# Performance work log

Hardware: AMD Instinct MI355X
Metric: run time of the kernel (lower is better)

Reference implementation:

```python
import jax, jax.numpy as jnp
import numpy as np

EPS = 1e-12  # torch F.normalize eps

def _l2norm(x):
    n = jnp.sqrt(jnp.sum(x * x, axis=-1, keepdims=True))
    return x / jnp.maximum(n, EPS)

def setup_inputs() -> dict:
    key = jax.random.key(0)
    k1, k2 = jax.random.split(key)
    B, C, H, W = 4, 256, 48, 48
    qkv = jax.random.normal(k1, (B, 3 * C, H, W), dtype=jnp.float32)
    temp = jnp.ones((8, 1, 1), dtype=jnp.float32)
    proj_w = jax.random.normal(k2, (C, C), dtype=jnp.float32) * (1.0 / np.sqrt(C))
    proj_b = jnp.zeros((C,), dtype=jnp.float32)
    return {"qkv": qkv, "temp": temp, "proj_w": proj_w, "proj_b": proj_b, "h": H, "w": W}

def reference(qkv, temp, proj_w, proj_b, h, w):
    num_heads = temp.shape[0]
    b = qkv.shape[0]
    q, k, v = jnp.split(qkv, 3, axis=1)

    def to_heads(x):
        # b (head c) h w -> b head (h w) c
        return x.reshape(b, num_heads, -1, h * w).transpose(0, 1, 3, 2)

    q = _l2norm(to_heads(q))
    k = _l2norm(to_heads(k))
    v = to_heads(v)

    # [b, head, N, N], temp (head,1,1) broadcasts over (n, m)
    attn = jnp.einsum('bhnc,bhmc->bhnm', q, k) * temp
    attn = jax.nn.softmax(jax.nn.relu(attn), axis=-1)
    out = jnp.einsum('bhnm,bhmc->bhnc', attn, v)
    # b head N c -> b head c N -> b (head c) h w
    out = out.transpose(0, 1, 3, 2).reshape(b, -1, h, w)
    # 1x1 conv == channel matmul
    out = jnp.einsum('oc,bchw->bohw', proj_w, out) + proj_b[None, :, None, None]
    return out
```

## Files before the change

### kernel.cpp

```cpp
#include <hip/hip_runtime.h>

typedef unsigned short u16;
typedef unsigned int   u32;
typedef __attribute__((ext_vector_type(8))) short short8;
typedef __attribute__((ext_vector_type(4))) float f32x4;

#define NB    4
#define NCH   256
#define NHD   8
#define HD    32
#define NSP   2304
#define NBH   32
#define NKT   36
#define KPW   9

__device__ __forceinline__ u16 f2bf(float f) {
    u32 u = __float_as_uint(f);
    u += 0x7FFFu + ((u >> 16) & 1u);
    return (u16)(u >> 16);
}
__device__ __forceinline__ u32 pack2(float a, float b) {
    return (u32)f2bf(a) | ((u32)f2bf(b) << 16);
}
__device__ __forceinline__ u32 pkfast(float a, float b) {
#if __has_builtin(__builtin_amdgcn_cvt_pk_bf16_f32)
    typedef __attribute__((ext_vector_type(2))) __bf16 bf2;
    union { bf2 v; u32 u; } cv;
    cv.v = __builtin_amdgcn_cvt_pk_bf16_f32(a, b);
    return cv.u;
#else
    return __builtin_amdgcn_perm(__float_as_uint(b), __float_as_uint(a), 0x07060302u);
#endif
}
__device__ __forceinline__ float fexp2(float x) {
#if __has_builtin(__builtin_amdgcn_exp2f)
    return __builtin_amdgcn_exp2f(x);
#else
    return exp2f(x);
#endif
}

__global__ __launch_bounds__(192) void prep_kernel(
    const float* __restrict__ qkv, const float* __restrict__ temp,
    const float* __restrict__ projw,
    u16* __restrict__ Qn, u16* __restrict__ Kn, u16* __restrict__ Vp,
    u16* __restrict__ Wb)
{
    const int p  = blockIdx.y;
    const int bh = blockIdx.z, b = bh >> 3, head = bh & 7;

    if (p == 3) {
        const int idx = (bh * 6 + blockIdx.x) * 192 + threadIdx.x;
        if (idx < NCH * NCH / 4) {
            float4 v = ((const float4*)projw)[idx];
            ((uint2*)Wb)[idx] = make_uint2(pack2(v.x, v.y), pack2(v.z, v.w));
        }
        return;
    }

    const int i  = blockIdx.x * 192 + threadIdx.x;
    const int n0 = i * 2;
    const float* src = qkv + ((size_t)(b * 3 * NCH + p * NCH + head * HD)) * NSP + n0;

    float2 v[HD];
#pragma unroll
    for (int d = 0; d < HD; ++d) v[d] = *(const float2*)(src + (size_t)d * NSP);

    if (p == 2) {
        const int tile = n0 >> 6, loc = n0 & 63;
        const int c = loc >> 5, r5 = loc & 31;
        const int qd  = (r5 < 16) ? (r5 >> 2) : ((r5 - 16) >> 2);
        const int jj  = (r5 < 16) ? (r5 & 3) : (4 + (r5 & 3));
        u16* dst = Vp + (size_t)bh * NSP * HD + (size_t)tile * 2048 + c * 32 + qd * 8 + jj;
#pragma unroll
        for (int d = 0; d < HD; ++d) *(u32*)(dst + d * 64) = pack2(v[d].x, v[d].y);
    } else {
        float s0 = 0.f, s1 = 0.f;
#pragma unroll
        for (int d = 0; d < HD; ++d) { s0 += v[d].x * v[d].x; s1 += v[d].y * v[d].y; }
        float sc0 = 1.f / fmaxf(sqrtf(s0), 1e-12f);
        float sc1 = 1.f / fmaxf(sqrtf(s1), 1e-12f);
        if (p == 0) {
            const float t = temp[head] * 1.44269504088896f;
            sc0 *= t; sc1 *= t;
        }
        u32 pk[HD];
#pragma unroll
        for (int j = 0; j < HD / 2; ++j) pk[j]          = pack2(v[2 * j].x * sc0, v[2 * j + 1].x * sc0);
#pragma unroll
        for (int j = 0; j < HD / 2; ++j) pk[HD / 2 + j] = pack2(v[2 * j].y * sc1, v[2 * j + 1].y * sc1);
        u16* dst = (p == 0 ? Qn : Kn) + ((size_t)bh * NSP + n0) * HD;
#pragma unroll
        for (int j = 0; j < 8; ++j) ((uint4*)dst)[j] = ((const uint4*)pk)[j];
    }
}

__global__ __launch_bounds__(256) void attn_kernel(
    const u16* __restrict__ Qn, const u16* __restrict__ Kn,
    const u16* __restrict__ Vp, u16* __restrict__ X)
{
    __shared__ float cmb[4][64][25];
    const int bh = blockIdx.x, b = bh >> 3, head = bh & 7;
    const int w = threadIdx.x >> 6, lane = threadIdx.x & 63;
    const int l15 = lane & 15, quad = lane >> 4;
    const int qbase = blockIdx.y * 64;

    const u16* Kg = Kn + (size_t)bh * NSP * HD + (size_t)w * KPW * 2048 + l15 * HD + quad * 8;
    const u16* Vg = Vp + (size_t)bh * NSP * HD + (size_t)w * KPW * 2048 + l15 * 64 + quad * 8;

    short8 qf[4];
#pragma unroll
    for (int t2 = 0; t2 < 4; ++t2)
        qf[t2] = *(const short8*)(Qn + ((size_t)bh * NSP + qbase + t2 * 16 + l15) * HD + quad * 8);

    const short one = (short)0x3F80;
    const short8 vones = {one, one, one, one, one, one, one, one};
    const f32x4 zf = {0.f, 0.f, 0.f, 0.f};

    f32x4 oacc[4][2] = {{{0,0,0,0},{0,0,0,0}},{{0,0,0,0},{0,0,0,0}},
                        {{0,0,0,0},{0,0,0,0}},{{0,0,0,0},{0,0,0,0}}};
    f32x4 rsac[4]    = {{0,0,0,0},{0,0,0,0},{0,0,0,0},{0,0,0,0}};

    short8 ka[4];
#pragma unroll
    for (int i = 0; i < 4; ++i) ka[i] = *(const short8*)(Kg + i * 512);

    for (int kt = 0; kt < KPW; ++kt) {
        short8 vb[2][2];
#pragma unroll
        for (int c = 0; c < 2; ++c)
#pragma unroll
            for (int h = 0; h < 2; ++h)
                vb[c][h] = *(const short8*)(Vg + (size_t)kt * 2048 + h * 1024 + c * 32);
        short8 kan[4];
        if (kt + 1 < KPW) {
            const u16* Kp2 = Kg + (size_t)(kt + 1) * 2048;
#pragma unroll
            for (int i = 0; i < 4; ++i) kan[i] = *(const short8*)(Kp2 + i * 512);
        }

#pragma unroll
        for (int t2 = 0; t2 < 4; ++t2) {
            f32x4 sf[4];
#pragma unroll
            for (int i = 0; i < 4; ++i)
                sf[i] = __builtin_amdgcn_mfma_f32_16x16x32_bf16(ka[i], qf[t2], zf, 0, 0, 0);
            u32 pk[4][2];
#pragma unroll
            for (int i = 0; i < 4; ++i) {
                pk[i][0] = pkfast(fexp2(fmaxf(sf[i][0], 0.f)), fexp2(fmaxf(sf[i][1], 0.f)));
                pk[i][1] = pkfast(fexp2(fmaxf(sf[i][2], 0.f)), fexp2(fmaxf(sf[i][3], 0.f)));
            }
#pragma unroll
            for (int c = 0; c < 2; ++c) {
                union { short8 s; u32 u[4]; } pa;
                pa.u[0] = pk[2 * c][0];     pa.u[1] = pk[2 * c][1];
                pa.u[2] = pk[2 * c + 1][0]; pa.u[3] = pk[2 * c + 1][1];
                oacc[t2][0] = __builtin_amdgcn_mfma_f32_16x16x32_bf16(pa.s, vb[c][0], oacc[t2][0], 0, 0, 0);
                oacc[t2][1] = __builtin_amdgcn_mfma_f32_16x16x32_bf16(pa.s, vb[c][1], oacc[t2][1], 0, 0, 0);
                rsac[t2]    = __builtin_amdgcn_mfma_f32_16x16x32_bf16(pa.s, vones,    rsac[t2],    0, 0, 0);
            }
        }

        if (kt + 1 < KPW) {
#pragma unroll
            for (int i = 0; i < 4; ++i) ka[i] = kan[i];
        }
    }

#pragma unroll
    for (int pass = 0; pass < 2; ++pass) {
        if (pass) __syncthreads();
        {
            float* my = &cmb[w][lane][0];
#pragma unroll
            for (int tt = 0; tt < 2; ++tt) {
                const int t2 = pass * 2 + tt;
#pragma unroll
                for (int h = 0; h < 2; ++h)
#pragma unroll
                    for (int r = 0; r < 4; ++r) my[tt * 12 + h * 4 + r] = oacc[t2][h][r];
#pragma unroll
                for (int r = 0; r < 4; ++r) my[tt * 12 + 8 + r] = rsac[t2][r];
            }
        }
        __syncthreads();
        if ((w >> 1) == pass) {
            const int t2 = w;
            const int tt = w & 1;
            float o0[4] = {0,0,0,0}, o1[4] = {0,0,0,0}, rsum[4] = {0,0,0,0};
#pragma unroll
            for (int j = 0; j < 4; ++j) {
                const float* srcp = &cmb[j][lane][tt * 12];
#pragma unroll
                for (int r = 0; r < 4; ++r) {
                    o0[r]   += srcp[r];
                    o1[r]   += srcp[4 + r];
                    rsum[r] += srcp[8 + r];
                }
            }
            u16* Xb = X + (size_t)b * NSP * NCH + head * HD;
#pragma unroll
            for (int r = 0; r < 4; ++r) {
                const float inv = 1.f / rsum[r];
                u16* row = Xb + (size_t)(qbase + t2 * 16 + quad * 4 + r) * NCH;
                row[l15]      = f2bf(o0[r] * inv);
                row[16 + l15] = f2bf(o1[r] * inv);
            }
        }
    }
}

__global__ __launch_bounds__(256) void proj_kernel(
    const u16* __restrict__ Wb, const u16* __restrict__ X,
    const float* __restrict__ bias, float* __restrict__ out)
{
    const int b = blockIdx.z;
    const int w = threadIdx.x >> 6, lane = threadIdx.x & 63;
    const int l15 = lane & 15, quad = lane >> 4;
    const int obase = blockIdx.y * 64 + w * 16;
    const int nbase = blockIdx.x * 32;

    const u16* wrow = Wb + (size_t)(obase + l15) * NCH + quad * 8;
    const u16* xrow = X + ((size_t)b * NSP + nbase + l15) * NCH + quad * 8;

    f32x4 acc[2] = {{0,0,0,0},{0,0,0,0}};
#pragma unroll
    for (int ks = 0; ks < 8; ++ks) {
        const short8 af = *(const short8*)(wrow + ks * 32);
        acc[0] = __builtin_amdgcn_mfma_f32_16x16x32_bf16(af, *(const short8*)(xrow + ks * 32), acc[0], 0, 0, 0);
        acc[1] = __builtin_amdgcn_mfma_f32_16x16x32_bf16(af, *(const short8*)(xrow + (size_t)16 * NCH + ks * 32), acc[1], 0, 0, 0);
    }
#pragma unroll
    for (int r = 0; r < 4; ++r) {
        const int o = obase + quad * 4 + r;
        const float bo = bias[o];
        float* orow = out + ((size_t)b * NCH + o) * NSP + nbase;
        orow[l15]      = acc[0][r] + bo;
        orow[16 + l15] = acc[1][r] + bo;
    }
}

extern "C" void kernel_launch(void* const* d_in, const int* in_sizes, int n_in,
                              void* d_out, int out_size, void* d_ws, size_t ws_size,
                              hipStream_t stream) {
    const float* qkv   = (const float*)d_in[0];
    const float* temp  = (const float*)d_in[1];
    const float* projw = (const float*)d_in[2];
    const float* projb = (const float*)d_in[3];
    float* out = (float*)d_out;

    u16* Qn = (u16*)d_ws;
    u16* Kn = Qn + (size_t)NBH * NSP * HD;
    u16* Vp = Kn + (size_t)NBH * NSP * HD;
    u16* X  = Vp + (size_t)NBH * NSP * HD;
    u16* Wb = X + (size_t)NB * NSP * NCH;

    prep_kernel<<<dim3(6, 4, NBH), dim3(192), 0, stream>>>(qkv, temp, projw, Qn, Kn, Vp, Wb);
    attn_kernel<<<dim3(NBH, NSP / 64), dim3(256), 0, stream>>>(Qn, Kn, Vp, X);
    proj_kernel<<<dim3(NSP / 32, NCH / 64, NB), dim3(256), 0, stream>>>(Wb, X, projb, out);
}
```

Baseline: 151.2 us.

## Split attention waves into query-pair by key-half instead of four key splits

```diff
diff --git a/kernel.cpp b/kernel.cpp
--- a/kernel.cpp
+++ b/kernel.cpp
@@ -12,7 +12,7 @@
 #define NSP   2304
 #define NBH   32
 #define NKT   36
-#define KPW   9
+#define KPW   18
 
 __device__ __forceinline__ u16 f2bf(float f) {
     u32 u = __float_as_uint(f);
@@ -39,6 +39,7 @@
     return exp2f(x);
 #endif
 }
+__device__ __forceinline__ float er(float x) { return fexp2(fmaxf(x, 0.f)); }
 
 __global__ __launch_bounds__(192) void prep_kernel(
     const float* __restrict__ qkv, const float* __restrict__ temp,
@@ -104,22 +105,22 @@
     const int w = threadIdx.x >> 6, lane = threadIdx.x & 63;
     const int l15 = lane & 15, quad = lane >> 4;
     const int qbase = blockIdx.y * 64;
-
-    const u16* Kg = Kn + (size_t)bh * NSP * HD + (size_t)w * KPW * 2048 + l15 * HD + quad * 8;
-    const u16* Vg = Vp + (size_t)bh * NSP * HD + (size_t)w * KPW * 2048 + l15 * 64 + quad * 8;
-
-    short8 qf[4];
-#pragma unroll
-    for (int t2 = 0; t2 < 4; ++t2)
-        qf[t2] = *(const short8*)(Qn + ((size_t)bh * NSP + qbase + t2 * 16 + l15) * HD + quad * 8);
+    const int qpair = w >> 1, khalf = w & 1;
+
+    const u16* Kg = Kn + (size_t)bh * NSP * HD + (size_t)khalf * KPW * 2048 + l15 * HD + quad * 8;
+    const u16* Vg = Vp + (size_t)bh * NSP * HD + (size_t)khalf * KPW * 2048 + l15 * 64 + quad * 8;
+
+    short8 qf[2];
+#pragma unroll
+    for (int t = 0; t < 2; ++t)
+        qf[t] = *(const short8*)(Qn + ((size_t)bh * NSP + qbase + (qpair * 2 + t) * 16 + l15) * HD + quad * 8);
 
     const short one = (short)0x3F80;
     const short8 vones = {one, one, one, one, one, one, one, one};
     const f32x4 zf = {0.f, 0.f, 0.f, 0.f};
 
-    f32x4 oacc[4][2] = {{{0,0,0,0},{0,0,0,0}},{{0,0,0,0},{0,0,0,0}},
-                        {{0,0,0,0},{0,0,0,0}},{{0,0,0,0},{0,0,0,0}}};
-    f32x4 rsac[4]    = {{0,0,0,0},{0,0,0,0},{0,0,0,0},{0,0,0,0}};
+    f32x4 oacc[2][2] = {{{0,0,0,0},{0,0,0,0}},{{0,0,0,0},{0,0,0,0}}};
+    f32x4 rsac[2]    = {{0,0,0,0},{0,0,0,0}};
 
     short8 ka[4];
 #pragma unroll
@@ -140,25 +141,21 @@
         }
 
 #pragma unroll
-        for (int t2 = 0; t2 < 4; ++t2) {
+        for (int t = 0; t < 2; ++t) {
             f32x4 sf[4];
 #pragma unroll
             for (int i = 0; i < 4; ++i)
-                sf[i] = __builtin_amdgcn_mfma_f32_16x16x32_bf16(ka[i], qf[t2], zf, 0, 0, 0);
-            u32 pk[4][2];
-#pragma unroll
-            for (int i = 0; i < 4; ++i) {
-                pk[i][0] = pkfast(fexp2(fmaxf(sf[i][0], 0.f)), fexp2(fmaxf(sf[i][1], 0.f)));
-                pk[i][1] = pkfast(fexp2(fmaxf(sf[i][2], 0.f)), fexp2(fmaxf(sf[i][3], 0.f)));
-            }
+                sf[i] = __builtin_amdgcn_mfma_f32_16x16x32_bf16(ka[i], qf[t], zf, 0, 0, 0);
 #pragma unroll
             for (int c = 0; c < 2; ++c) {
                 union { short8 s; u32 u[4]; } pa;
-                pa.u[0] = pk[2 * c][0];     pa.u[1] = pk[2 * c][1];
-                pa.u[2] = pk[2 * c + 1][0]; pa.u[3] = pk[2 * c + 1][1];
-                oacc[t2][0] = __builtin_amdgcn_mfma_f32_16x16x32_bf16(pa.s, vb[c][0], oacc[t2][0], 0, 0, 0);
-                oacc[t2][1] = __builtin_amdgcn_mfma_f32_16x16x32_bf16(pa.s, vb[c][1], oacc[t2][1], 0, 0, 0);
-                rsac[t2]    = __builtin_amdgcn_mfma_f32_16x16x32_bf16(pa.s, vones,    rsac[t2],    0, 0, 0);
+                pa.u[0] = pkfast(er(sf[2 * c][0]),     er(sf[2 * c][1]));
+                pa.u[1] = pkfast(er(sf[2 * c][2]),     er(sf[2 * c][3]));
+                pa.u[2] = pkfast(er(sf[2 * c + 1][0]), er(sf[2 * c + 1][1]));
+                pa.u[3] = pkfast(er(sf[2 * c + 1][2]), er(sf[2 * c + 1][3]));
+                oacc[t][0] = __builtin_amdgcn_mfma_f32_16x16x32_bf16(pa.s, vb[c][0], oacc[t][0], 0, 0, 0);
+                oacc[t][1] = __builtin_amdgcn_mfma_f32_16x16x32_bf16(pa.s, vb[c][1], oacc[t][1], 0, 0, 0);
+                rsac[t]    = __builtin_amdgcn_mfma_f32_16x16x32_bf16(pa.s, vones,    rsac[t],    0, 0, 0);
             }
         }
 
@@ -168,45 +165,39 @@
         }
     }
 
-#pragma unroll
-    for (int pass = 0; pass < 2; ++pass) {
-        if (pass) __syncthreads();
-        {
-            float* my = &cmb[w][lane][0];
-#pragma unroll
-            for (int tt = 0; tt < 2; ++tt) {
-                const int t2 = pass * 2 + tt;
-#pragma unroll
-                for (int h = 0; h < 2; ++h)
-#pragma unroll
-                    for (int r = 0; r < 4; ++r) my[tt * 12 + h * 4 + r] = oacc[t2][h][r];
-#pragma unroll
-                for (int r = 0; r < 4; ++r) my[tt * 12 + 8 + r] = rsac[t2][r];
-            }
-        }
-        __syncthreads();
-        if ((w >> 1) == pass) {
-            const int t2 = w;
-            const int tt = w & 1;
-            float o0[4] = {0,0,0,0}, o1[4] = {0,0,0,0}, rsum[4] = {0,0,0,0};
-#pragma unroll
-            for (int j = 0; j < 4; ++j) {
-                const float* srcp = &cmb[j][lane][tt * 12];
-#pragma unroll
-                for (int r = 0; r < 4; ++r) {
-                    o0[r]   += srcp[r];
-                    o1[r]   += srcp[4 + r];
-                    rsum[r] += srcp[8 + r];
-                }
-            }
-            u16* Xb = X + (size_t)b * NSP * NCH + head * HD;
-#pragma unroll
-            for (int r = 0; r < 4; ++r) {
-                const float inv = 1.f / rsum[r];
-                u16* row = Xb + (size_t)(qbase + t2 * 16 + quad * 4 + r) * NCH;
-                row[l15]      = f2bf(o0[r] * inv);
-                row[16 + l15] = f2bf(o1[r] * inv);
-            }
+    {
+        float* my = &cmb[w][lane][0];
+#pragma unroll
+        for (int tt = 0; tt < 2; ++tt) {
+#pragma unroll
+            for (int h = 0; h < 2; ++h)
+#pragma unroll
+                for (int r = 0; r < 4; ++r) my[tt * 12 + h * 4 + r] = oacc[tt][h][r];
+#pragma unroll
+            for (int r = 0; r < 4; ++r) my[tt * 12 + 8 + r] = rsac[tt][r];
+        }
+    }
+    __syncthreads();
+    {
+        const int t2 = w;
+        const int jbase = w & ~1;
+        const int tt = w & 1;
+        float o0[4], o1[4], rsum[4];
+        const float* s0p = &cmb[jbase][lane][tt * 12];
+        const float* s1p = &cmb[jbase + 1][lane][tt * 12];
+#pragma unroll
+        for (int r = 0; r < 4; ++r) {
+            o0[r]   = s0p[r]     + s1p[r];
+            o1[r]   = s0p[4 + r] + s1p[4 + r];
+            rsum[r] = s0p[8 + r] + s1p[8 + r];
+        }
+        u16* Xb = X + (size_t)b * NSP * NCH + head * HD;
+#pragma unroll
+        for (int r = 0; r < 4; ++r) {
+            const float inv = 1.f / rsum[r];
+            u16* row = Xb + (size_t)(qbase + t2 * 16 + quad * 4 + r) * NCH;
+            row[l15]      = f2bf(o0[r] * inv);
+            row[16 + l15] = f2bf(o1[r] * inv);
         }
     }
 }
```

New measurement: 166.6 us. +10.2%, slower.

## Unroll attention key loop with ping-pong K registers, MFMA priority, single-pass reduce

Applied to the files above, without the earlier changes.

```diff
diff --git a/kernel.cpp b/kernel.cpp
--- a/kernel.cpp
+++ b/kernel.cpp
@@ -39,6 +39,7 @@
     return exp2f(x);
 #endif
 }
+__device__ __forceinline__ float er(float x) { return fexp2(fmaxf(x, 0.f)); }
 
 __global__ __launch_bounds__(192) void prep_kernel(
     const float* __restrict__ qkv, const float* __restrict__ temp,
@@ -95,11 +96,60 @@
     }
 }
 
+__device__ __forceinline__ void kbody(
+    const u16* __restrict__ Kg, const u16* __restrict__ Vg, int kt, bool pf,
+    short8 (&kc)[4], short8 (&kn)[4], const short8 (&qf)[4],
+    f32x4 (&oacc)[4][2], f32x4 (&rsac)[4])
+{
+    const short one = (short)0x3F80;
+    const short8 vones = {one, one, one, one, one, one, one, one};
+    const f32x4 zf = {0.f, 0.f, 0.f, 0.f};
+
+    short8 vb[2][2];
+#pragma unroll
+    for (int c = 0; c < 2; ++c)
+#pragma unroll
+        for (int h = 0; h < 2; ++h)
+            vb[c][h] = *(const short8*)(Vg + (size_t)kt * 2048 + h * 1024 + c * 32);
+    if (pf) {
+#pragma unroll
+        for (int i = 0; i < 4; ++i)
+            kn[i] = *(const short8*)(Kg + (size_t)(kt + 1) * 2048 + i * 512);
+    }
+
+#pragma unroll
+    for (int t2 = 0; t2 < 4; ++t2) {
+        f32x4 sf[4];
+        __builtin_amdgcn_s_setprio(1);
+#pragma unroll
+        for (int i = 0; i < 4; ++i)
+            sf[i] = __builtin_amdgcn_mfma_f32_16x16x32_bf16(kc[i], qf[t2], zf, 0, 0, 0);
+        __builtin_amdgcn_s_setprio(0);
+        u32 pk[4][2];
+#pragma unroll
+        for (int i = 0; i < 4; ++i) {
+            pk[i][0] = pkfast(er(sf[i][0]), er(sf[i][1]));
+            pk[i][1] = pkfast(er(sf[i][2]), er(sf[i][3]));
+        }
+#pragma unroll
+        for (int c = 0; c < 2; ++c) {
+            union { short8 s; u32 u[4]; } pa;
+            pa.u[0] = pk[2 * c][0];     pa.u[1] = pk[2 * c][1];
+            pa.u[2] = pk[2 * c + 1][0]; pa.u[3] = pk[2 * c + 1][1];
+            __builtin_amdgcn_s_setprio(1);
+            oacc[t2][0] = __builtin_amdgcn_mfma_f32_16x16x32_bf16(pa.s, vb[c][0], oacc[t2][0], 0, 0, 0);
+            oacc[t2][1] = __builtin_amdgcn_mfma_f32_16x16x32_bf16(pa.s, vb[c][1], oacc[t2][1], 0, 0, 0);
+            rsac[t2]    = __builtin_amdgcn_mfma_f32_16x16x32_bf16(pa.s, vones,    rsac[t2],    0, 0, 0);
+            __builtin_amdgcn_s_setprio(0);
+        }
+    }
+}
+
 __global__ __launch_bounds__(256) void attn_kernel(
     const u16* __restrict__ Qn, const u16* __restrict__ Kn,
     const u16* __restrict__ Vp, u16* __restrict__ X)
 {
-    __shared__ float cmb[4][64][25];
+    __shared__ float cmb[4][64][49];
     const int bh = blockIdx.x, b = bh >> 3, head = bh & 7;
     const int w = threadIdx.x >> 6, lane = threadIdx.x & 63;
     const int l15 = lane & 15, quad = lane >> 4;
@@ -113,100 +163,53 @@
     for (int t2 = 0; t2 < 4; ++t2)
         qf[t2] = *(const short8*)(Qn + ((size_t)bh * NSP + qbase + t2 * 16 + l15) * HD + quad * 8);
 
-    const short one = (short)0x3F80;
-    const short8 vones = {one, one, one, one, one, one, one, one};
-    const f32x4 zf = {0.f, 0.f, 0.f, 0.f};
-
     f32x4 oacc[4][2] = {{{0,0,0,0},{0,0,0,0}},{{0,0,0,0},{0,0,0,0}},
                         {{0,0,0,0},{0,0,0,0}},{{0,0,0,0},{0,0,0,0}}};
     f32x4 rsac[4]    = {{0,0,0,0},{0,0,0,0},{0,0,0,0},{0,0,0,0}};
 
-    short8 ka[4];
+    short8 ka[4], kb[4];
 #pragma unroll
     for (int i = 0; i < 4; ++i) ka[i] = *(const short8*)(Kg + i * 512);
 
-    for (int kt = 0; kt < KPW; ++kt) {
-        short8 vb[2][2];
-#pragma unroll
-        for (int c = 0; c < 2; ++c)
+    for (int kt = 0; kt < KPW - 1; kt += 2) {
+        kbody(Kg, Vg, kt,     true,  ka, kb, qf, oacc, rsac);
+        kbody(Kg, Vg, kt + 1, true,  kb, ka, qf, oacc, rsac);
+    }
+    kbody(Kg, Vg, KPW - 1, false, ka, kb, qf, oacc, rsac);
+
+    {
+        float* my = &cmb[w][lane][0];
+#pragma unroll
+        for (int t2 = 0; t2 < 4; ++t2) {
 #pragma unroll
             for (int h = 0; h < 2; ++h)
-                vb[c][h] = *(const short8*)(Vg + (size_t)kt * 2048 + h * 1024 + c * 32);
-        short8 kan[4];
-        if (kt + 1 < KPW) {
-            const u16* Kp2 = Kg + (size_t)(kt + 1) * 2048;
-#pragma unroll
-            for (int i = 0; i < 4; ++i) kan[i] = *(const short8*)(Kp2 + i * 512);
-        }
-
-#pragma unroll
-        for (int t2 = 0; t2 < 4; ++t2) {
-            f32x4 sf[4];
-#pragma unroll
-            for (int i = 0; i < 4; ++i)
-                sf[i] = __builtin_amdgcn_mfma_f32_16x16x32_bf16(ka[i], qf[t2], zf, 0, 0, 0);
-            u32 pk[4][2];
-#pragma unroll
-            for (int i = 0; i < 4; ++i) {
-                pk[i][0] = pkfast(fexp2(fmaxf(sf[i][0], 0.f)), fexp2(fmaxf(sf[i][1], 0.f)));
-                pk[i][1] = pkfast(fexp2(fmaxf(sf[i][2], 0.f)), fexp2(fmaxf(sf[i][3], 0.f)));
+#pragma unroll
+                for (int r = 0; r < 4; ++r) my[t2 * 12 + h * 4 + r] = oacc[t2][h][r];
+#pragma unroll
+            for (int r = 0; r < 4; ++r) my[t2 * 12 + 8 + r] = rsac[t2][r];
+        }
+    }
+    __syncthreads();
+    {
+        const int t2 = w;
+        float o0[4] = {0,0,0,0}, o1[4] = {0,0,0,0}, rsum[4] = {0,0,0,0};
+#pragma unroll
+        for (int j = 0; j < 4; ++j) {
+            const float* srcp = &cmb[j][lane][t2 * 12];
+#pragma unroll
+            for (int r = 0; r < 4; ++r) {
+                o0[r]   += srcp[r];
+                o1[r]   += srcp[4 + r];
+                rsum[r] += srcp[8 + r];
             }
-#pragma unroll
-            for (int c = 0; c < 2; ++c) {
-                union { short8 s; u32 u[4]; } pa;
-                pa.u[0] = pk[2 * c][0];     pa.u[1] = pk[2 * c][1];
-                pa.u[2] = pk[2 * c + 1][0]; pa.u[3] = pk[2 * c + 1][1];
-                oacc[t2][0] = __builtin_amdgcn_mfma_f32_16x16x32_bf16(pa.s, vb[c][0], oacc[t2][0], 0, 0, 0);
-                oacc[t2][1] = __builtin_amdgcn_mfma_f32_16x16x32_bf16(pa.s, vb[c][1], oacc[t2][1], 0, 0, 0);
-                rsac[t2]    = __builtin_amdgcn_mfma_f32_16x16x32_bf16(pa.s, vones,    rsac[t2],    0, 0, 0);
-            }
-        }
-
-        if (kt + 1 < KPW) {
-#pragma unroll
-            for (int i = 0; i < 4; ++i) ka[i] = kan[i];
-        }
-    }
-
-#pragma unroll
-    for (int pass = 0; pass < 2; ++pass) {
-        if (pass) __syncthreads();
-        {
-            float* my = &cmb[w][lane][0];
-#pragma unroll
-            for (int tt = 0; tt < 2; ++tt) {
-                const int t2 = pass * 2 + tt;
-#pragma unroll
-                for (int h = 0; h < 2; ++h)
-#pragma unroll
-                    for (int r = 0; r < 4; ++r) my[tt * 12 + h * 4 + r] = oacc[t2][h][r];
-#pragma unroll
-                for (int r = 0; r < 4; ++r) my[tt * 12 + 8 + r] = rsac[t2][r];
-            }
-        }
-        __syncthreads();
-        if ((w >> 1) == pass) {
-            const int t2 = w;
-            const int tt = w & 1;
-            float o0[4] = {0,0,0,0}, o1[4] = {0,0,0,0}, rsum[4] = {0,0,0,0};
-#pragma unroll
-            for (int j = 0; j < 4; ++j) {
-                const float* srcp = &cmb[j][lane][tt * 12];
-#pragma unroll
-                for (int r = 0; r < 4; ++r) {
-                    o0[r]   += srcp[r];
-                    o1[r]   += srcp[4 + r];
-                    rsum[r] += srcp[8 + r];
-                }
-            }
-            u16* Xb = X + (size_t)b * NSP * NCH + head * HD;
-#pragma unroll
-            for (int r = 0; r < 4; ++r) {
-                const float inv = 1.f / rsum[r];
-                u16* row = Xb + (size_t)(qbase + t2 * 16 + quad * 4 + r) * NCH;
-                row[l15]      = f2bf(o0[r] * inv);
-                row[16 + l15] = f2bf(o1[r] * inv);
-            }
+        }
+        u16* Xb = X + (size_t)b * NSP * NCH + head * HD;
+#pragma unroll
+        for (int r = 0; r < 4; ++r) {
+            const float inv = 1.f / rsum[r];
+            u16* row = Xb + (size_t)(qbase + t2 * 16 + quad * 4 + r) * NCH;
+            row[l15]      = f2bf(o0[r] * inv);
+            row[16 + l15] = f2bf(o1[r] * inv);
         }
     }
 }
```

Measured after the change: 148.6 us. No clear change (-1.7%).
